# Performance work log

Hardware: AMD Instinct MI355X
Metric: run time of the kernel (lower is better)

Reference implementation:

```python
import jax, jax.numpy as jnp
import numpy as np

VOCAB = 28996
B, W, D, H = 16, 64, 256, 512


def setup_inputs() -> dict:
    key = jax.random.key(0)
    ks = jax.random.split(key, 8)
    s_ih = 1.0 / np.sqrt(H)
    return {
        "x": jax.random.normal(ks[0], (B, W, D), dtype=jnp.float32),
        "last_encoder_hidden_state": jax.random.normal(ks[1], (1, H), dtype=jnp.float32),
        "w_ih": jax.random.uniform(ks[2], (3 * H, D), jnp.float32, -s_ih, s_ih),
        "w_hh": jax.random.uniform(ks[3], (3 * H, H), jnp.float32, -s_ih, s_ih),
        "b_ih": jax.random.uniform(ks[4], (3 * H,), jnp.float32, -s_ih, s_ih),
        "b_hh": jax.random.uniform(ks[5], (3 * H,), jnp.float32, -s_ih, s_ih),
        "w_pred": jax.random.uniform(ks[6], (VOCAB, H), jnp.float32, -s_ih, s_ih),
        "b_pred": jax.random.uniform(ks[7], (VOCAB,), jnp.float32, -s_ih, s_ih),
    }


def reference(x, last_encoder_hidden_state, w_ih, w_hh, b_ih, b_hh, w_pred, b_pred):
    b, w, d = x.shape
    # The torch code carries a single [1,H] hidden state sequentially over ALL
    # batch rows and words (state flows across batch boundaries). Flatten to T steps.
    xf = x.reshape(b * w, d)
    xg = xf @ w_ih.T + b_ih  # [T, 3H] input gate pre-activations, batched GEMM

    def step(h, xg_t):
        gh = h @ w_hh.T + b_hh            # [3H]
        xr, xz, xn = jnp.split(xg_t, 3)
        hr, hz, hn = jnp.split(gh, 3)
        r = jax.nn.sigmoid(xr + hr)
        z = jax.nn.sigmoid(xz + hz)
        n = jnp.tanh(xn + r * hn)
        h_new = (1.0 - z) * n + z * h
        return h_new, h_new

    h0 = last_encoder_hidden_state[0]     # [H]
    _, hs = jax.lax.scan(step, h0, xg)    # hs: [T, H]
    preds = hs @ w_pred.T + b_pred        # [T, VOCAB]
    return preds.reshape(b, w, VOCAB)
```

## Files before the change

### kernel.cpp

```cpp
#include <hip/hip_runtime.h>
#include <hip/hip_bf16.h>
#include <cstdint>

#define VOCAB 28996
#define T_STEPS 1024
#define D_IN 256
#define HDIM 512

using f32x4 = __attribute__((ext_vector_type(4))) float;
using s16x8 = __attribute__((ext_vector_type(8))) short;

static __device__ __forceinline__ unsigned short f2bf(float f){
    unsigned u = __float_as_uint(f);
    u = u + 0x7FFFu + ((u >> 16) & 1u);
    return (unsigned short)(u >> 16);
}

#define SENT_U 0x7FC00001u

__global__ void init_hs_kernel(const float* __restrict__ h0, float* __restrict__ hs,
                               unsigned* __restrict__ ctrl){
    const int col = threadIdx.x;
    const int row = blockIdx.x;
    float v = (row == 0) ? h0[col] : __uint_as_float(SENT_U);
    hs[(size_t)row * HDIM + col] = v;
    if (row == 0 && col < 8) ctrl[col] = 0u;
}

__global__ void xg_kernel(const float* __restrict__ x, const float* __restrict__ w_ih,
                          const float* __restrict__ b_ih, float* __restrict__ xg){
    __shared__ float xs[8][D_IN];
    const int tid = threadIdx.x;
    const int i   = blockIdx.x * 256 + tid;
    const int t0  = blockIdx.y * 8;
    #pragma unroll
    for (int r = 0; r < 8; ++r)
        xs[r][tid] = x[(size_t)(t0 + r) * D_IN + tid];
    __syncthreads();

    float acc[8] = {0.f,0.f,0.f,0.f,0.f,0.f,0.f,0.f};
    const float* wrow = w_ih + (size_t)i * D_IN;
    for (int d = 0; d < D_IN; d += 4){
        float4 w4 = *(const float4*)(wrow + d);
        #pragma unroll
        for (int r = 0; r < 8; ++r){
            acc[r] += w4.x * xs[r][d]   + w4.y * xs[r][d+1]
                    + w4.z * xs[r][d+2] + w4.w * xs[r][d+3];
        }
    }
    const float b = b_ih[i];
    #pragma unroll
    for (int r = 0; r < 8; ++r)
        xg[(size_t)(t0 + r) * (3*HDIM) + i] = acc[r] + b;
}

#define LDW(G, P, n) \
    float G##n##0 = (P)[64*n + 0], G##n##1 = (P)[64*n + 1], \
          G##n##2 = (P)[64*n + 2], G##n##3 = (P)[64*n + 3];
#define PINW(G, n) \
    asm volatile("" : "+v"(G##n##0), "+v"(G##n##1), "+v"(G##n##2), "+v"(G##n##3));

#define GSTEP(n, arx, azx, anx) { \
    float4 h4 = *(const float4*)&hbuf[wv][4*c + 64*n]; \
    arx += R##n##0*h4.x + R##n##1*h4.y + R##n##2*h4.z + R##n##3*h4.w; \
    azx += Z##n##0*h4.x + Z##n##1*h4.y + Z##n##2*h4.z + Z##n##3*h4.w; \
    anx += N##n##0*h4.x + N##n##1*h4.y + N##n##2*h4.z + N##n##3*h4.w; }

__launch_bounds__(512)
__attribute__((amdgpu_waves_per_eu(2, 2)))
__global__ void scan_kernel(const float* __restrict__ xg, const float* __restrict__ w_hh,
                            const float* __restrict__ b_hh, float* hs, unsigned* ctrl){
    __shared__ __align__(16) float hbuf[8][HDIM];
    __shared__ unsigned sh_rank;

    const int tid = threadIdx.x;
    if (tid == 0){
        unsigned xcc;
        asm volatile("s_getreg_b32 %0, hwreg(HW_REG_XCC_ID)" : "=s"(xcc));
        sh_rank = __hip_atomic_fetch_add(&ctrl[xcc & 7u], 1u, __ATOMIC_RELAXED,
                                         __HIP_MEMORY_SCOPE_AGENT);
    }
    __syncthreads();
    const unsigned rank = sh_rank;
    if (rank >= 16u) return;

    const int wv   = tid >> 6;
    const int lane = tid & 63;
    const int c    = tid & 15;
    const int jl   = tid >> 4;
    const int j    = (int)rank * 32 + jl;

    const float* wrp = w_hh + (size_t)j * HDIM + 4*c;
    const float* wzp = w_hh + (size_t)(HDIM   + j) * HDIM + 4*c;
    const float* wnp = w_hh + (size_t)(2*HDIM + j) * HDIM + 4*c;
    LDW(R, wrp, 0) LDW(R, wrp, 1) LDW(R, wrp, 2) LDW(R, wrp, 3)
    LDW(R, wrp, 4) LDW(R, wrp, 5) LDW(R, wrp, 6) LDW(R, wrp, 7)
    LDW(Z, wzp, 0) LDW(Z, wzp, 1) LDW(Z, wzp, 2) LDW(Z, wzp, 3)
    LDW(Z, wzp, 4) LDW(Z, wzp, 5) LDW(Z, wzp, 6) LDW(Z, wzp, 7)
    LDW(N, wnp, 0) LDW(N, wnp, 1) LDW(N, wnp, 2) LDW(N, wnp, 3)
    LDW(N, wnp, 4) LDW(N, wnp, 5) LDW(N, wnp, 6) LDW(N, wnp, 7)
    PINW(R,0) PINW(R,1) PINW(R,2) PINW(R,3) PINW(R,4) PINW(R,5) PINW(R,6) PINW(R,7)
    PINW(Z,0) PINW(Z,1) PINW(Z,2) PINW(Z,3) PINW(Z,4) PINW(Z,5) PINW(Z,6) PINW(Z,7)
    PINW(N,0) PINW(N,1) PINW(N,2) PINW(N,3) PINW(N,4) PINW(N,5) PINW(N,6) PINW(N,7)

    float bhr = b_hh[j], bhz = b_hh[HDIM + j], bhn = b_hh[2*HDIM + j];
    asm volatile("" : "+v"(bhr), "+v"(bhz), "+v"(bhn));

    float xr_c = 0.f, xz_c = 0.f, xn_c = 0.f;
    if (c == 0){ xr_c = xg[j]; xz_c = xg[HDIM + j]; xn_c = xg[2*HDIM + j]; }

    #pragma unroll 1
    for (int t = 0; t < T_STEPS; ++t){
        const float4* myp = (const float4*)(hs + (size_t)t * HDIM) + lane;
        float4 va, vb;
        int spins = 0;
        for (;;){
            asm volatile("global_load_dwordx4 %0, %2, off nt\n\t"
                         "global_load_dwordx4 %1, %2, off offset:1024 nt\n\t"
                         "s_waitcnt vmcnt(0)"
                         : "=&v"(va), "=&v"(vb) : "v"(myp) : "memory");
            int ok = (__float_as_uint(va.x) != SENT_U) & (__float_as_uint(va.y) != SENT_U)
                   & (__float_as_uint(va.z) != SENT_U) & (__float_as_uint(va.w) != SENT_U)
                   & (__float_as_uint(vb.x) != SENT_U) & (__float_as_uint(vb.y) != SENT_U)
                   & (__float_as_uint(vb.z) != SENT_U) & (__float_as_uint(vb.w) != SENT_U);
            if (__all(ok)) break;
            if (++spins > 5000) return;
        }

        float xr_n = 0.f, xz_n = 0.f, xn_n = 0.f;
        if (c == 0 && t + 1 < T_STEPS){
            const float* xgn = xg + (size_t)(t + 1) * (3*HDIM);
            xr_n = xgn[j]; xz_n = xgn[HDIM + j]; xn_n = xgn[2*HDIM + j];
        }

        *(float4*)&hbuf[wv][4 * lane]       = va;
        *(float4*)&hbuf[wv][256 + 4 * lane] = vb;
        asm volatile("s_waitcnt lgkmcnt(0)" ::: "memory");
        __builtin_amdgcn_sched_barrier(0);

        float ar0=0.f, ar1=0.f, az0=0.f, az1=0.f, an0=0.f, an1=0.f;
        GSTEP(0, ar0, az0, an0)  GSTEP(1, ar1, az1, an1)
        GSTEP(2, ar0, az0, an0)  GSTEP(3, ar1, az1, an1)
        GSTEP(4, ar0, az0, an0)  GSTEP(5, ar1, az1, an1)
        GSTEP(6, ar0, az0, an0)  GSTEP(7, ar1, az1, an1)
        float ar = ar0 + ar1, az = az0 + az1, an = an0 + an1;
        #pragma unroll
        for (int m = 1; m < 16; m <<= 1){
            ar += __shfl_xor(ar, m);
            az += __shfl_xor(az, m);
            an += __shfl_xor(an, m);
        }

        if (c == 0){
            const float r  = 1.0f / (1.0f + __expf(-(xr_c + ar + bhr)));
            const float z  = 1.0f / (1.0f + __expf(-(xz_c + az + bhz)));
            const float nn = xn_c + r * (an + bhn);
            const float e  = __expf(2.0f * nn);
            const float th = 1.0f - 2.0f / (e + 1.0f);
            const float hnew = (1.0f - z) * th + z * hbuf[wv][j];
            hs[(size_t)(t + 1) * HDIM + j] = hnew;
        }
        asm volatile("s_waitcnt vmcnt(0)" ::: "memory");

        xr_c = xr_n; xz_c = xz_n; xn_c = xn_n;
    }
}

__launch_bounds__(256)
__global__ void pred_gemm_kernel(const float* __restrict__ hs, const float* __restrict__ w_pred,
                                 const float* __restrict__ b_pred, float* __restrict__ out){
    __shared__ unsigned short As[128 * 32];
    __shared__ unsigned short Bs[128 * 32];
    const int tid   = threadIdx.x;
    const int mtile = blockIdx.x;
    const int ntile = blockIdx.y;
    const int row  = tid >> 1, half = tid & 1;
    const int wave = tid >> 6, lane = tid & 63;
    const int wm = wave >> 1, wn = wave & 1;
    const int lr = lane & 15, kq = lane >> 4;

    f32x4 acc[4][4] = {};

    const float* Abase = hs + HDIM  + (size_t)(mtile * 128 + row) * HDIM;
    const int    nrow  = ntile * 128 + row;
    const float* Bbase = w_pred + (size_t)nrow * HDIM;

    for (int k0 = 0; k0 < HDIM; k0 += 32){
        {
            const float* srcp = Abase + k0 + half * 16;
            unsigned short* dst = &As[row * 32 + half * 16];
            #pragma unroll
            for (int q = 0; q < 4; ++q){
                float4 v = *(const float4*)(srcp + 4 * q);
                uint2 p;
                p.x = (unsigned)f2bf(v.x) | ((unsigned)f2bf(v.y) << 16);
                p.y = (unsigned)f2bf(v.z) | ((unsigned)f2bf(v.w) << 16);
                *(uint2*)(dst + 4 * q) = p;
            }
        }
        {
            unsigned short* dst = &Bs[row * 32 + half * 16];
            if (nrow < VOCAB){
                const float* srcp = Bbase + k0 + half * 16;
                #pragma unroll
                for (int q = 0; q < 4; ++q){
                    float4 v = *(const float4*)(srcp + 4 * q);
                    uint2 p;
                    p.x = (unsigned)f2bf(v.x) | ((unsigned)f2bf(v.y) << 16);
                    p.y = (unsigned)f2bf(v.z) | ((unsigned)f2bf(v.w) << 16);
                    *(uint2*)(dst + 4 * q) = p;
                }
            } else {
                uint2 zz; zz.x = 0u; zz.y = 0u;
                #pragma unroll
                for (int q = 0; q < 4; ++q) *(uint2*)(dst + 4 * q) = zz;
            }
        }
        __syncthreads();

        const unsigned short* Ab = &As[(wm * 64 + lr) * 32 + kq * 8];
        const unsigned short* Bb = &Bs[(wn * 64 + lr) * 32 + kq * 8];
        s16x8 af[4], bf[4];
        #pragma unroll
        for (int mf = 0; mf < 4; ++mf) af[mf] = *(const s16x8*)(Ab + mf * 16 * 32);
        #pragma unroll
        for (int nf = 0; nf < 4; ++nf) bf[nf] = *(const s16x8*)(Bb + nf * 16 * 32);
        #pragma unroll
        for (int mf = 0; mf < 4; ++mf){
            #pragma unroll
            for (int nf = 0; nf < 4; ++nf){
                acc[mf][nf] = __builtin_amdgcn_mfma_f32_16x16x32_bf16(af[mf], bf[nf], acc[mf][nf], 0, 0, 0);
            }
        }
        __syncthreads();
    }

    #pragma unroll
    for (int nf = 0; nf < 4; ++nf){
        const int n = ntile * 128 + wn * 64 + nf * 16 + lr;
        if (n >= VOCAB) continue;
        const float bp = b_pred[n];
        #pragma unroll
        for (int mf = 0; mf < 4; ++mf){
            const int m = mtile * 128 + wm * 64 + mf * 16 + kq * 4;
            #pragma unroll
            for (int q = 0; q < 4; ++q){
                out[(size_t)(m + q) * VOCAB + n] = acc[mf][nf][q] + bp;
            }
        }
    }
}

extern "C" void kernel_launch(void* const* d_in, const int* in_sizes, int n_in,
                              void* d_out, int out_size, void* d_ws, size_t ws_size,
                              hipStream_t stream){
    const float* x      = (const float*)d_in[0];
    const float* h0     = (const float*)d_in[1];
    const float* w_ih   = (const float*)d_in[2];
    const float* w_hh   = (const float*)d_in[3];
    const float* b_ih   = (const float*)d_in[4];
    const float* b_hh   = (const float*)d_in[5];
    const float* w_pred = (const float*)d_in[6];
    const float* b_pred = (const float*)d_in[7];
    float* out = (float*)d_out;

    float*    xg   = (float*)d_ws;
    float*    hs   = xg + (size_t)T_STEPS * (3*HDIM);
    unsigned* ctrl = (unsigned*)(hs + (size_t)(T_STEPS+1) * HDIM);

    hipLaunchKernelGGL(init_hs_kernel, dim3(T_STEPS + 1), dim3(HDIM), 0, stream, h0, hs, ctrl);
    hipLaunchKernelGGL(xg_kernel,      dim3(6, 128),      dim3(256),  0, stream, x, w_ih, b_ih, xg);
    hipLaunchKernelGGL(scan_kernel,    dim3(128),         dim3(512),  0, stream, xg, w_hh, b_hh, hs, ctrl);
    hipLaunchKernelGGL(pred_gemm_kernel, dim3(8, 227),    dim3(256),  0, stream, hs, w_pred, b_pred, out);
}
```

Baseline: 1.665 ms.

## Split GRU scan across 32 workgroups with 16 hidden units each

Redistributes the recurrent matvec so each workgroup owns 16 hidden units and each unit is reduced by 32 lanes, doubling the number of active scan workgroups. Each thread holds fewer w_hh registers and does fewer FMAs per step, shortening the per-step critical path. In exchange, the shuffle reduction gains one more level and twice as many blocks poll the shared hidden-state buffer every step, which may increase synchronisation contention.

Result: faster. 1.567 ms (-5.9%).

```diff
diff --git a/kernel.cpp b/kernel.cpp
--- a/kernel.cpp
+++ b/kernel.cpp
@@ -54,17 +54,17 @@
         xg[(size_t)(t0 + r) * (3*HDIM) + i] = acc[r] + b;
 }
 
-#define LDW(G, P, n) \
-    float G##n##0 = (P)[64*n + 0], G##n##1 = (P)[64*n + 1], \
-          G##n##2 = (P)[64*n + 2], G##n##3 = (P)[64*n + 3];
-#define PINW(G, n) \
-    asm volatile("" : "+v"(G##n##0), "+v"(G##n##1), "+v"(G##n##2), "+v"(G##n##3));
-
-#define GSTEP(n, arx, azx, anx) { \
-    float4 h4 = *(const float4*)&hbuf[wv][4*c + 64*n]; \
-    arx += R##n##0*h4.x + R##n##1*h4.y + R##n##2*h4.z + R##n##3*h4.w; \
-    azx += Z##n##0*h4.x + Z##n##1*h4.y + Z##n##2*h4.z + Z##n##3*h4.w; \
-    anx += N##n##0*h4.x + N##n##1*h4.y + N##n##2*h4.z + N##n##3*h4.w; }
+#define LDW(G, P, s) \
+    float G##s##0 = (P)[128*s + 0], G##s##1 = (P)[128*s + 1], \
+          G##s##2 = (P)[128*s + 2], G##s##3 = (P)[128*s + 3];
+#define PINW(G, s) \
+    asm volatile("" : "+v"(G##s##0), "+v"(G##s##1), "+v"(G##s##2), "+v"(G##s##3));
+
+#define GSTEP(s) { \
+    float4 h4 = *(const float4*)&hbuf[wv][4*c + 128*s]; \
+    ar += R##s##0*h4.x + R##s##1*h4.y + R##s##2*h4.z + R##s##3*h4.w; \
+    az += Z##s##0*h4.x + Z##s##1*h4.y + Z##s##2*h4.z + Z##s##3*h4.w; \
+    an += N##s##0*h4.x + N##s##1*h4.y + N##s##2*h4.z + N##s##3*h4.w; }
 
 __launch_bounds__(512)
 __attribute__((amdgpu_waves_per_eu(2, 2)))
@@ -82,26 +82,23 @@
     }
     __syncthreads();
     const unsigned rank = sh_rank;
-    if (rank >= 16u) return;
+    if (rank >= 32u) return;
 
     const int wv   = tid >> 6;
     const int lane = tid & 63;
-    const int c    = tid & 15;
-    const int jl   = tid >> 4;
-    const int j    = (int)rank * 32 + jl;
+    const int c    = tid & 31;
+    const int jl   = tid >> 5;
+    const int j    = (int)rank * 16 + jl;
 
     const float* wrp = w_hh + (size_t)j * HDIM + 4*c;
     const float* wzp = w_hh + (size_t)(HDIM   + j) * HDIM + 4*c;
     const float* wnp = w_hh + (size_t)(2*HDIM + j) * HDIM + 4*c;
     LDW(R, wrp, 0) LDW(R, wrp, 1) LDW(R, wrp, 2) LDW(R, wrp, 3)
-    LDW(R, wrp, 4) LDW(R, wrp, 5) LDW(R, wrp, 6) LDW(R, wrp, 7)
     LDW(Z, wzp, 0) LDW(Z, wzp, 1) LDW(Z, wzp, 2) LDW(Z, wzp, 3)
-    LDW(Z, wzp, 4) LDW(Z, wzp, 5) LDW(Z, wzp, 6) LDW(Z, wzp, 7)
     LDW(N, wnp, 0) LDW(N, wnp, 1) LDW(N, wnp, 2) LDW(N, wnp, 3)
-    LDW(N, wnp, 4) LDW(N, wnp, 5) LDW(N, wnp, 6) LDW(N, wnp, 7)
-    PINW(R,0) PINW(R,1) PINW(R,2) PINW(R,3) PINW(R,4) PINW(R,5) PINW(R,6) PINW(R,7)
-    PINW(Z,0) PINW(Z,1) PINW(Z,2) PINW(Z,3) PINW(Z,4) PINW(Z,5) PINW(Z,6) PINW(Z,7)
-    PINW(N,0) PINW(N,1) PINW(N,2) PINW(N,3) PINW(N,4) PINW(N,5) PINW(N,6) PINW(N,7)
+    PINW(R,0) PINW(R,1) PINW(R,2) PINW(R,3)
+    PINW(Z,0) PINW(Z,1) PINW(Z,2) PINW(Z,3)
+    PINW(N,0) PINW(N,1) PINW(N,2) PINW(N,3)
 
     float bhr = b_hh[j], bhz = b_hh[HDIM + j], bhn = b_hh[2*HDIM + j];
     asm volatile("" : "+v"(bhr), "+v"(bhz), "+v"(bhn));
@@ -138,14 +135,10 @@
         asm volatile("s_waitcnt lgkmcnt(0)" ::: "memory");
         __builtin_amdgcn_sched_barrier(0);
 
-        float ar0=0.f, ar1=0.f, az0=0.f, az1=0.f, an0=0.f, an1=0.f;
-        GSTEP(0, ar0, az0, an0)  GSTEP(1, ar1, az1, an1)
-        GSTEP(2, ar0, az0, an0)  GSTEP(3, ar1, az1, an1)
-        GSTEP(4, ar0, az0, an0)  GSTEP(5, ar1, az1, an1)
-        GSTEP(6, ar0, az0, an0)  GSTEP(7, ar1, az1, an1)
-        float ar = ar0 + ar1, az = az0 + az1, an = an0 + an1;
-        #pragma unroll
-        for (int m = 1; m < 16; m <<= 1){
+        float ar = 0.f, az = 0.f, an = 0.f;
+        GSTEP(0) GSTEP(1) GSTEP(2) GSTEP(3)
+        #pragma unroll
+        for (int m = 1; m < 32; m <<= 1){
             ar += __shfl_xor(ar, m);
             az += __shfl_xor(az, m);
             an += __shfl_xor(an, m);
@@ -270,6 +263,6 @@
 
     hipLaunchKernelGGL(init_hs_kernel, dim3(T_STEPS + 1), dim3(HDIM), 0, stream, h0, hs, ctrl);
     hipLaunchKernelGGL(xg_kernel,      dim3(6, 128),      dim3(256),  0, stream, x, w_ih, b_ih, xg);
-    hipLaunchKernelGGL(scan_kernel,    dim3(128),         dim3(512),  0, stream, xg, w_hh, b_hh, hs, ctrl);
+    hipLaunchKernelGGL(scan_kernel,    dim3(256),         dim3(512),  0, stream, xg, w_hh, b_hh, hs, ctrl);
     hipLaunchKernelGGL(pred_gemm_kernel, dim3(8, 227),    dim3(256),  0, stream, hs, w_pred, b_pred, out);
 }
```
